# Optimization experiments

Hardware: AMD Instinct MI355X
Metric: run time of the kernel (lower is better)

The kernel has to match this reference:

```python
import jax, jax.numpy as jnp
import numpy as np

DIM = 32  # fixed internal node dim
N_GRAPHS = 64


def setup_inputs() -> dict:
    key = jax.random.key(0)
    ks = jax.random.split(key, 16)
    N, E, F_N, F_E, H = 12500, 200000, 16, 8, 32
    inp = {
        "x": jax.random.normal(ks[0], (N, F_N), dtype=jnp.float32),
        "edge_index": jax.random.randint(ks[1], (2, E), 0, N, dtype=jnp.int64),
        "edge_attr": jax.random.normal(ks[2], (E, F_E), dtype=jnp.float32),
        "batch": jnp.sort(jax.random.randint(ks[3], (N,), 0, N_GRAPHS, dtype=jnp.int64)),
        "lin0_w": jax.random.normal(ks[4], (DIM, F_N), dtype=jnp.float32) * 0.1,
        "lin0_b": jax.random.normal(ks[5], (DIM,), dtype=jnp.float32) * 0.1,
        "nn_w": jax.random.normal(ks[6], (DIM * H, F_E), dtype=jnp.float32) * 0.1,
        "nn_b": jax.random.normal(ks[7], (DIM * H,), dtype=jnp.float32) * 0.1,
        "root_w": jax.random.normal(ks[8], (DIM, H), dtype=jnp.float32) * 0.1,
        "conv_b": jax.random.normal(ks[9], (H,), dtype=jnp.float32) * 0.1,
        "lin1_w": jax.random.normal(ks[10], (16, H), dtype=jnp.float32) * 0.1,
        "lin1_b": jax.random.normal(ks[11], (16,), dtype=jnp.float32) * 0.1,
        "lin2_w": jax.random.normal(ks[12], (1, 16), dtype=jnp.float32) * 0.1,
        "lin2_b": jax.random.normal(ks[13], (1,), dtype=jnp.float32) * 0.1,
    }
    return inp


def reference(x, edge_index, edge_attr, batch, lin0_w, lin0_b, nn_w, nn_b,
              root_w, conv_b, lin1_w, lin1_b, lin2_w, lin2_b):
    N = x.shape[0]
    H = conv_b.shape[0]
    # lin0 + relu -> node features [N, DIM]
    out = jax.nn.relu(x @ lin0_w.T + lin0_b)
    # NNConv: per-edge weight matrices from edge MLP (single Linear)
    src, dst = edge_index[0], edge_index[1]
    w_e = (edge_attr @ nn_w.T + nn_b).reshape(-1, DIM, H)  # [E, DIM, H]
    msg = jnp.einsum('ed,edh->eh', out[src], w_e)          # gather + per-edge matmul
    agg = jax.ops.segment_sum(msg, dst, num_segments=N)     # scatter-add
    h = jax.nn.relu(agg + out @ root_w + conv_b)             # root weight + bias
    # global add pool over graphs
    u = jax.ops.segment_sum(h, batch, num_segments=N_GRAPHS)  # [G, H]
    o = jax.nn.relu(u @ lin1_w.T + lin1_b)
    o = o @ lin2_w.T + lin2_b
    return o.reshape(-1)
```

## Files before the change

kernel.cpp:

```cpp
#include <hip/hip_runtime.h>

#define DIMN 32
#define HD   32
#define FN   16
#define FE   8
#define NG   64
#define CAP  64
#define NPW  2
#define K3T  512
#define K3W  (K3T / 64)
#define K3NPB (K3W * NPW)

__global__ __launch_bounds__(256) void k1_out(
    const float* __restrict__ x, const float* __restrict__ lin0_w,
    const float* __restrict__ lin0_b,
    float* __restrict__ outn, float* __restrict__ aggfb, float* __restrict__ u,
    int* __restrict__ deg, int N)
{
    const int gt = blockIdx.x * 256 + threadIdx.x;
    if (gt >= N * DIMN) return;
    const int n = gt >> 5, d = gt & 31;

    float s = lin0_b[d];
    const float* xr = x + (size_t)n * FN;
    const float* wr = lin0_w + d * FN;
    #pragma unroll
    for (int j = 0; j < FN; ++j) s = fmaf(xr[j], wr[j], s);
    outn[gt] = fmaxf(s, 0.f);

    aggfb[gt] = 0.f;
    if (d == 0) deg[n] = 0;
    if (gt < NG * HD) u[gt] = 0.f;
}

__global__ __launch_bounds__(256) void kb_bucket(
    const int* __restrict__ ei, const float* __restrict__ ea,
    const float* __restrict__ outn, const float* __restrict__ nn_w,
    const float* __restrict__ nn_b,
    int* __restrict__ deg, int2* __restrict__ es, float* __restrict__ aggfb, int E)
{
    const int e = blockIdx.x * 256 + threadIdx.x;
    if (e >= E) return;
    const int src = ei[e];
    const int dst = ei[E + e];
    const int pos = atomicAdd(&deg[dst], 1);
    if (pos < CAP) {
        es[(size_t)dst * CAP + pos] = make_int2(e, src);
    } else {
        float ef[FE];
        #pragma unroll
        for (int f = 0; f < FE; ++f) ef[f] = ea[(size_t)e * FE + f];
        for (int h = 0; h < HD; ++h) {
            float m = 0.f;
            for (int d = 0; d < DIMN; ++d) {
                float wdh = nn_b[d * HD + h];
                #pragma unroll
                for (int f = 0; f < FE; ++f)
                    wdh = fmaf(ef[f], nn_w[(d * HD + h) * FE + f], wdh);
                m = fmaf(outn[(size_t)src * DIMN + d], wdh, m);
            }
            atomicAdd(aggfb + (size_t)dst * HD + h, m);
        }
    }
}

__global__ __launch_bounds__(K3T) void k3_gather(
    const float* __restrict__ ea, const float* __restrict__ outn,
    const int2* __restrict__ es, const float* __restrict__ nn_w,
    const float* __restrict__ nn_b, const float* __restrict__ root_w,
    const float* __restrict__ conv_b, const int* __restrict__ deg,
    const float* __restrict__ aggfb, const int* __restrict__ batch,
    float* __restrict__ u, int N)
{
    __shared__ float s_nnw2[DIMN * FE * HD];
    __shared__ float s_nnb[DIMN * HD];
    __shared__ float s_rw[DIMN * HD];
    __shared__ float s_cb[HD];
    __shared__ float s_T[K3W * 256];
    __shared__ float s_S[K3W * 32];
    __shared__ float s_O[K3W * 32];

    const int tid = threadIdx.x;
    for (int i = tid; i < DIMN * FE * HD; i += K3T) {
        const int d = i >> 8, rem = i & 255, hh = rem >> 3, f = rem & 7;
        s_nnw2[(d * 8 + f) * 32 + hh] = nn_w[i];
    }
    for (int i = tid; i < DIMN * HD; i += K3T) { s_nnb[i] = nn_b[i]; s_rw[i] = root_w[i]; }
    if (tid < HD) s_cb[tid] = conv_b[tid];
    __syncthreads();

    const int l = tid & 63;
    const int h = l & 31;
    const int p = l >> 5;
    const int w = tid >> 6;
    const int wid   = blockIdx.x * K3W + w;
    const int nbase = wid * NPW;

    float accp  = 0.f;
    int   g_cur = -1;

    for (int i = 0; i < NPW; ++i) {
        const int n = nbase + i;
        if (n >= N) break;
        const int nu = __builtin_amdgcn_readfirstlane(n);
        const int dn = min(deg[nu], CAP);
        const int2* ep = es + (size_t)nu * CAP;

        float T0a = 0.f, T1a = 0.f, T2a = 0.f, T3a = 0.f, Sa = 0.f;
        float T0b = 0.f, T1b = 0.f, T2b = 0.f, T3b = 0.f, Sb = 0.f;
        int j = 0;
        for (; j + 2 <= dn; j += 2) {
            const int2 eA = ep[j];
            const int2 eB = ep[j + 1];
            const float4 wA = *(const float4*)(ea + (size_t)eA.x * FE + 4 * p);
            const float4 wB = *(const float4*)(ea + (size_t)eB.x * FE + 4 * p);
            const float  oA = outn[(size_t)eA.y * DIMN + h];
            const float  oB = outn[(size_t)eB.y * DIMN + h];
            Sa += oA;  Sb += oB;
            T0a = fmaf(oA, wA.x, T0a);  T1a = fmaf(oA, wA.y, T1a);
            T2a = fmaf(oA, wA.z, T2a);  T3a = fmaf(oA, wA.w, T3a);
            T0b = fmaf(oB, wB.x, T0b);  T1b = fmaf(oB, wB.y, T1b);
            T2b = fmaf(oB, wB.z, T2b);  T3b = fmaf(oB, wB.w, T3b);
        }
        if (j < dn) {
            const int2 eA = ep[j];
            const float4 wA = *(const float4*)(ea + (size_t)eA.x * FE + 4 * p);
            const float  oA = outn[(size_t)eA.y * DIMN + h];
            Sa += oA;
            T0a = fmaf(oA, wA.x, T0a);  T1a = fmaf(oA, wA.y, T1a);
            T2a = fmaf(oA, wA.z, T2a);  T3a = fmaf(oA, wA.w, T3a);
        }
        const float4 tv = make_float4(T0a + T0b, T1a + T1b, T2a + T2b, T3a + T3b);

        *(float4*)&s_T[w * 256 + h * 8 + 4 * p] = tv;
        if (p == 0) {
            s_S[w * 32 + h] = Sa + Sb;
            s_O[w * 32 + h] = outn[(size_t)nu * DIMN + h];
        }

        float acc = 0.f;
        const int d0 = p << 4;
        #pragma unroll
        for (int dd = 0; dd < 16; ++dd) {
            const int d = d0 + dd;
            const float4 ta = *(const float4*)&s_T[w * 256 + d * 8];
            const float4 tb = *(const float4*)&s_T[w * 256 + d * 8 + 4];
            const int base = d * 256 + h;
            acc = fmaf(ta.x, s_nnw2[base +   0], acc);
            acc = fmaf(ta.y, s_nnw2[base +  32], acc);
            acc = fmaf(ta.z, s_nnw2[base +  64], acc);
            acc = fmaf(ta.w, s_nnw2[base +  96], acc);
            acc = fmaf(tb.x, s_nnw2[base + 128], acc);
            acc = fmaf(tb.y, s_nnw2[base + 160], acc);
            acc = fmaf(tb.z, s_nnw2[base + 192], acc);
            acc = fmaf(tb.w, s_nnw2[base + 224], acc);
            acc = fmaf(s_S[w * 32 + d], s_nnb[d * 32 + h], acc);
            acc = fmaf(s_O[w * 32 + d], s_rw [d * 32 + h], acc);
        }
        acc += __shfl_xor(acc, 32);

        const float v = fmaxf(acc + s_cb[h] + aggfb[(size_t)n * HD + h], 0.f);

        const int g = batch[nu];
        if (g != g_cur) {
            if (g_cur >= 0 && p == 0) atomicAdd(u + (size_t)g_cur * HD + h, accp);
            g_cur = g;
            accp = v;
        } else {
            accp += v;
        }
    }
    if (g_cur >= 0 && p == 0) atomicAdd(u + (size_t)g_cur * HD + h, accp);
}

__global__ __launch_bounds__(64) void k4_head(
    const float* __restrict__ u, const float* __restrict__ lin1_w,
    const float* __restrict__ lin1_b, const float* __restrict__ lin2_w,
    const float* __restrict__ lin2_b, float* __restrict__ outp)
{
    const int g = threadIdx.x;
    if (g >= NG) return;

    float ur[HD];
    #pragma unroll
    for (int hh = 0; hh < HD; ++hh) ur[hh] = u[(size_t)g * HD + hh];

    float acc = lin2_b[0];
    #pragma unroll
    for (int i = 0; i < 16; ++i) {
        float o = lin1_b[i];
        #pragma unroll
        for (int hh = 0; hh < HD; ++hh)
            o = fmaf(ur[hh], lin1_w[i * HD + hh], o);
        o = fmaxf(o, 0.f);
        acc = fmaf(o, lin2_w[i], acc);
    }
    outp[g] = acc;
}

extern "C" void kernel_launch(void* const* d_in, const int* in_sizes, int n_in,
                              void* d_out, int out_size, void* d_ws, size_t ws_size,
                              hipStream_t stream)
{
    const float* x      = (const float*)d_in[0];
    const int*   ei     = (const int*)  d_in[1];
    const float* ea     = (const float*)d_in[2];
    const int*   batch  = (const int*)  d_in[3];
    const float* lin0_w = (const float*)d_in[4];
    const float* lin0_b = (const float*)d_in[5];
    const float* nn_w   = (const float*)d_in[6];
    const float* nn_b   = (const float*)d_in[7];
    const float* root_w = (const float*)d_in[8];
    const float* conv_b = (const float*)d_in[9];
    const float* lin1_w = (const float*)d_in[10];
    const float* lin1_b = (const float*)d_in[11];
    const float* lin2_w = (const float*)d_in[12];
    const float* lin2_b = (const float*)d_in[13];

    const int N = in_sizes[0] / FN;
    const int E = in_sizes[2] / FE;

    float* ws    = (float*)d_ws;
    float* outn  = ws;
    float* aggfb = outn  + (size_t)N * DIMN;
    float* u     = aggfb + (size_t)N * DIMN;
    int*   deg   = (int*)(u + (size_t)NG * HD);
    int2*  es    = (int2*)(deg + N);

    const int nb1 = (N * DIMN + 255) / 256;
    k1_out<<<nb1, 256, 0, stream>>>(x, lin0_w, lin0_b, outn, aggfb, u, deg, N);

    const int nbb = (E + 255) / 256;
    kb_bucket<<<nbb, 256, 0, stream>>>(ei, ea, outn, nn_w, nn_b, deg, es, aggfb, E);

    const int nb3 = (N + K3NPB - 1) / K3NPB;
    k3_gather<<<nb3, K3T, 0, stream>>>(ea, outn, es, nn_w, nn_b, root_w, conv_b,
                                       deg, aggfb, batch, u, N);

    k4_head<<<1, 64, 0, stream>>>(u, lin1_w, lin1_b, lin2_w, lin2_b, (float*)d_out);
}
```

Before: 166.2 us.

## Use one node per wave, unroll edge gather by 8, reduce pooling in-block

```diff
diff --git a/kernel.cpp b/kernel.cpp
--- a/kernel.cpp
+++ b/kernel.cpp
@@ -6,10 +6,8 @@
 #define FE   8
 #define NG   64
 #define CAP  64
-#define NPW  2
 #define K3T  512
 #define K3W  (K3T / 64)
-#define K3NPB (K3W * NPW)
 
 __global__ __launch_bounds__(256) void k1_out(
     const float* __restrict__ x, const float* __restrict__ lin0_w,
@@ -64,7 +62,31 @@
     }
 }
 
-__global__ __launch_bounds__(K3T) void k3_gather(
+#define EDGE_FMA(o, a) \
+    S  = (S + (o));                      \
+    T0 = fmaf((o), (a).x, T0);           \
+    T1 = fmaf((o), (a).y, T1);           \
+    T2 = fmaf((o), (a).z, T2);           \
+    T3 = fmaf((o), (a).w, T3);
+
+#define CONTRIB(DD, A) { \
+    const int d_ = d0 + (DD); \
+    const float4 ta_ = *(const float4*)&s_T[w * 256 + d_ * 8]; \
+    const float4 tb_ = *(const float4*)&s_T[w * 256 + d_ * 8 + 4]; \
+    const float2 so_ = s_SO[w * 32 + d_]; \
+    const int b_ = d_ * 256 + h; \
+    A = fmaf(ta_.x, s_nnw2[b_      ], A); \
+    A = fmaf(ta_.y, s_nnw2[b_ +  32], A); \
+    A = fmaf(ta_.z, s_nnw2[b_ +  64], A); \
+    A = fmaf(ta_.w, s_nnw2[b_ +  96], A); \
+    A = fmaf(tb_.x, s_nnw2[b_ + 128], A); \
+    A = fmaf(tb_.y, s_nnw2[b_ + 160], A); \
+    A = fmaf(tb_.z, s_nnw2[b_ + 192], A); \
+    A = fmaf(tb_.w, s_nnw2[b_ + 224], A); \
+    A = fmaf(so_.x, s_nnb[d_ * 32 + h], A); \
+    A = fmaf(so_.y, s_rw [d_ * 32 + h], A); }
+
+__global__ __launch_bounds__(K3T, 8) void k3_gather(
     const float* __restrict__ ea, const float* __restrict__ outn,
     const int2* __restrict__ es, const float* __restrict__ nn_w,
     const float* __restrict__ nn_b, const float* __restrict__ root_w,
@@ -72,13 +94,14 @@
     const float* __restrict__ aggfb, const int* __restrict__ batch,
     float* __restrict__ u, int N)
 {
-    __shared__ float s_nnw2[DIMN * FE * HD];
-    __shared__ float s_nnb[DIMN * HD];
-    __shared__ float s_rw[DIMN * HD];
-    __shared__ float s_cb[HD];
-    __shared__ float s_T[K3W * 256];
-    __shared__ float s_S[K3W * 32];
-    __shared__ float s_O[K3W * 32];
+    __shared__ float  s_nnw2[DIMN * FE * HD];
+    __shared__ float  s_nnb[DIMN * HD];
+    __shared__ float  s_rw[DIMN * HD];
+    __shared__ float  s_cb[HD];
+    __shared__ float  s_T[K3W * 256];
+    __shared__ float2 s_SO[K3W * 32];
+    __shared__ float  s_V[K3W * 32];
+    __shared__ int    s_G[K3W];
 
     const int tid = threadIdx.x;
     for (int i = tid; i < DIMN * FE * HD; i += K3T) {
@@ -93,84 +116,100 @@
     const int h = l & 31;
     const int p = l >> 5;
     const int w = tid >> 6;
-    const int wid   = blockIdx.x * K3W + w;
-    const int nbase = wid * NPW;
-
-    float accp  = 0.f;
-    int   g_cur = -1;
-
-    for (int i = 0; i < NPW; ++i) {
-        const int n = nbase + i;
-        if (n >= N) break;
+    const int n = blockIdx.x * K3W + w;
+
+    int gval = -1;
+    if (n < N) {
         const int nu = __builtin_amdgcn_readfirstlane(n);
         const int dn = min(deg[nu], CAP);
         const int2* ep = es + (size_t)nu * CAP;
-
-        float T0a = 0.f, T1a = 0.f, T2a = 0.f, T3a = 0.f, Sa = 0.f;
-        float T0b = 0.f, T1b = 0.f, T2b = 0.f, T3b = 0.f, Sb = 0.f;
-        int j = 0;
-        for (; j + 2 <= dn; j += 2) {
-            const int2 eA = ep[j];
-            const int2 eB = ep[j + 1];
-            const float4 wA = *(const float4*)(ea + (size_t)eA.x * FE + 4 * p);
-            const float4 wB = *(const float4*)(ea + (size_t)eB.x * FE + 4 * p);
-            const float  oA = outn[(size_t)eA.y * DIMN + h];
-            const float  oB = outn[(size_t)eB.y * DIMN + h];
-            Sa += oA;  Sb += oB;
-            T0a = fmaf(oA, wA.x, T0a);  T1a = fmaf(oA, wA.y, T1a);
-            T2a = fmaf(oA, wA.z, T2a);  T3a = fmaf(oA, wA.w, T3a);
-            T0b = fmaf(oB, wB.x, T0b);  T1b = fmaf(oB, wB.y, T1b);
-            T2b = fmaf(oB, wB.z, T2b);  T3b = fmaf(oB, wB.w, T3b);
-        }
-        if (j < dn) {
-            const int2 eA = ep[j];
-            const float4 wA = *(const float4*)(ea + (size_t)eA.x * FE + 4 * p);
-            const float  oA = outn[(size_t)eA.y * DIMN + h];
-            Sa += oA;
-            T0a = fmaf(oA, wA.x, T0a);  T1a = fmaf(oA, wA.y, T1a);
-            T2a = fmaf(oA, wA.z, T2a);  T3a = fmaf(oA, wA.w, T3a);
-        }
-        const float4 tv = make_float4(T0a + T0b, T1a + T1b, T2a + T2b, T3a + T3b);
-
-        *(float4*)&s_T[w * 256 + h * 8 + 4 * p] = tv;
-        if (p == 0) {
-            s_S[w * 32 + h] = Sa + Sb;
-            s_O[w * 32 + h] = outn[(size_t)nu * DIMN + h];
-        }
-
-        float acc = 0.f;
+        const int f0 = 4 * p;
+
+        float T0 = 0.f, T1 = 0.f, T2 = 0.f, T3 = 0.f, S = 0.f;
+
+        for (int j0 = 0; j0 < dn; j0 += 8) {
+            const int jm = dn - 1;
+            const int2 E0 = ep[j0];
+            const int2 E1 = ep[min(j0 + 1, jm)];
+            const int2 E2 = ep[min(j0 + 2, jm)];
+            const int2 E3 = ep[min(j0 + 3, jm)];
+            const int2 E4 = ep[min(j0 + 4, jm)];
+            const int2 E5 = ep[min(j0 + 5, jm)];
+            const int2 E6 = ep[min(j0 + 6, jm)];
+            const int2 E7 = ep[min(j0 + 7, jm)];
+
+            const float4 a0 = *(const float4*)(ea + (size_t)E0.x * FE + f0);
+            const float4 a1 = *(const float4*)(ea + (size_t)E1.x * FE + f0);
+            const float4 a2 = *(const float4*)(ea + (size_t)E2.x * FE + f0);
+            const float4 a3 = *(const float4*)(ea + (size_t)E3.x * FE + f0);
+            const float4 a4 = *(const float4*)(ea + (size_t)E4.x * FE + f0);
+            const float4 a5 = *(const float4*)(ea + (size_t)E5.x * FE + f0);
+            const float4 a6 = *(const float4*)(ea + (size_t)E6.x * FE + f0);
+            const float4 a7 = *(const float4*)(ea + (size_t)E7.x * FE + f0);
+            float o0 = outn[(size_t)E0.y * DIMN + h];
+            float o1 = outn[(size_t)E1.y * DIMN + h];
+            float o2 = outn[(size_t)E2.y * DIMN + h];
+            float o3 = outn[(size_t)E3.y * DIMN + h];
+            float o4 = outn[(size_t)E4.y * DIMN + h];
+            float o5 = outn[(size_t)E5.y * DIMN + h];
+            float o6 = outn[(size_t)E6.y * DIMN + h];
+            float o7 = outn[(size_t)E7.y * DIMN + h];
+
+            o1 = (j0 + 1 <= jm) ? o1 : 0.f;
+            o2 = (j0 + 2 <= jm) ? o2 : 0.f;
+            o3 = (j0 + 3 <= jm) ? o3 : 0.f;
+            o4 = (j0 + 4 <= jm) ? o4 : 0.f;
+            o5 = (j0 + 5 <= jm) ? o5 : 0.f;
+            o6 = (j0 + 6 <= jm) ? o6 : 0.f;
+            o7 = (j0 + 7 <= jm) ? o7 : 0.f;
+
+            EDGE_FMA(o0, a0) EDGE_FMA(o1, a1) EDGE_FMA(o2, a2) EDGE_FMA(o3, a3)
+            EDGE_FMA(o4, a4) EDGE_FMA(o5, a5) EDGE_FMA(o6, a6) EDGE_FMA(o7, a7)
+        }
+
+        *(float4*)&s_T[w * 256 + h * 8 + f0] = make_float4(T0, T1, T2, T3);
+        if (p == 0) s_SO[w * 32 + h] = make_float2(S, outn[(size_t)nu * DIMN + h]);
+
+        const float base = aggfb[(size_t)nu * HD + h] + s_cb[h];
+
+        float acc0 = 0.f, acc1 = 0.f, acc2 = 0.f, acc3 = 0.f;
         const int d0 = p << 4;
         #pragma unroll
-        for (int dd = 0; dd < 16; ++dd) {
-            const int d = d0 + dd;
-            const float4 ta = *(const float4*)&s_T[w * 256 + d * 8];
-            const float4 tb = *(const float4*)&s_T[w * 256 + d * 8 + 4];
-            const int base = d * 256 + h;
-            acc = fmaf(ta.x, s_nnw2[base +   0], acc);
-            acc = fmaf(ta.y, s_nnw2[base +  32], acc);
-            acc = fmaf(ta.z, s_nnw2[base +  64], acc);
-            acc = fmaf(ta.w, s_nnw2[base +  96], acc);
-            acc = fmaf(tb.x, s_nnw2[base + 128], acc);
-            acc = fmaf(tb.y, s_nnw2[base + 160], acc);
-            acc = fmaf(tb.z, s_nnw2[base + 192], acc);
-            acc = fmaf(tb.w, s_nnw2[base + 224], acc);
-            acc = fmaf(s_S[w * 32 + d], s_nnb[d * 32 + h], acc);
-            acc = fmaf(s_O[w * 32 + d], s_rw [d * 32 + h], acc);
-        }
+        for (int dd = 0; dd < 16; dd += 4) {
+            CONTRIB(dd + 0, acc0)
+            CONTRIB(dd + 1, acc1)
+            CONTRIB(dd + 2, acc2)
+            CONTRIB(dd + 3, acc3)
+        }
+        float acc = (acc0 + acc1) + (acc2 + acc3);
         acc += __shfl_xor(acc, 32);
 
-        const float v = fmaxf(acc + s_cb[h] + aggfb[(size_t)n * HD + h], 0.f);
-
-        const int g = batch[nu];
-        if (g != g_cur) {
-            if (g_cur >= 0 && p == 0) atomicAdd(u + (size_t)g_cur * HD + h, accp);
-            g_cur = g;
-            accp = v;
-        } else {
-            accp += v;
-        }
-    }
-    if (g_cur >= 0 && p == 0) atomicAdd(u + (size_t)g_cur * HD + h, accp);
+        const float v = fmaxf(acc + base, 0.f);
+        if (p == 0) s_V[w * 32 + h] = v;
+        gval = batch[nu];
+    }
+    if (l == 0) s_G[w] = gval;
+    __syncthreads();
+
+    if (tid < 32) {
+        float accp = 0.f;
+        int   gc   = -1;
+        #pragma unroll
+        for (int ww = 0; ww < K3W; ++ww) {
+            const int gg = s_G[ww];
+            if (gg >= 0) {
+                const float vv = s_V[ww * 32 + tid];
+                if (gg != gc) {
+                    if (gc >= 0) atomicAdd(u + (size_t)gc * HD + tid, accp);
+                    gc = gg;
+                    accp = vv;
+                } else {
+                    accp += vv;
+                }
+            }
+        }
+        if (gc >= 0) atomicAdd(u + (size_t)gc * HD + tid, accp);
+    }
 }
 
 __global__ __launch_bounds__(64) void k4_head(
@@ -233,7 +272,7 @@
     const int nbb = (E + 255) / 256;
     kb_bucket<<<nbb, 256, 0, stream>>>(ei, ea, outn, nn_w, nn_b, deg, es, aggfb, E);
 
-    const int nb3 = (N + K3NPB - 1) / K3NPB;
+    const int nb3 = (N + K3W - 1) / K3W;
     k3_gather<<<nb3, K3T, 0, stream>>>(ea, outn, es, nn_w, nn_b, root_w, conv_b,
                                        deg, aggfb, batch, u, N);
 
```

Result: faster. 141.7 us (-14.7%).
